# Optimization experiments

Measured on AMD Instinct MI355X. Metric: run time of the kernel, lower is better.

The kernel has to match this reference:

```python
import jax, jax.numpy as jnp
import numpy as np

N, C, H, W, Z = 2, 12, 128, 128, 128
SMOOTH = 1e-5  # MONAI DiceLoss smooth_nr / smooth_dr defaults
BETA = 3.0


def setup_inputs() -> dict:
    key = jax.random.key(0)
    k1, k2, k3 = jax.random.split(key, 3)
    inp = jax.random.normal(k1, (N, C, H, W, Z), dtype=jnp.float32)
    tgt = jax.random.randint(k2, (N, 1, H, W, Z), 0, C, dtype=jnp.int64)
    mat = jax.random.uniform(k3, (C, C), dtype=jnp.float32)
    return {"input": inp, "target": tgt, "matrix_penalty": mat}


def reference(input, target, matrix_penalty):
    c = input.shape[1]
    tgt = target[:, 0]  # (n,h,w,z) integer labels

    # ---- CE part of DiceCELoss (softmax cross-entropy, mean reduction) ----
    logp = jax.nn.log_softmax(input, axis=1)            # (n,c,h,w,z)
    ce = -jnp.mean(jnp.take_along_axis(logp, target, axis=1))

    # ---- Dice part (to_onehot_y=True, softmax=True, include_background) ----
    p = jnp.exp(logp)                                    # softmax probs
    t1h = jax.nn.one_hot(tgt, c, axis=1, dtype=p.dtype)  # (n,c,h,w,z)
    axes = (2, 3, 4)                                     # reduce spatial dims
    inter = jnp.sum(t1h * p, axis=axes)                  # (n,c)
    ground_o = jnp.sum(t1h, axis=axes)
    pred_o = jnp.sum(p, axis=axes)
    dice = jnp.mean(1.0 - (2.0 * inter + SMOOTH) / (ground_o + pred_o + SMOOTH))

    # ---- DOMINO penalty: mean over pixels of M[t,:] . softmax(logits) ----
    rows = matrix_penalty[tgt]                           # (n,h,w,z,c) gather
    p_last = jnp.moveaxis(p, 1, -1)                      # (n,h,w,z,c)
    penalty = BETA * jnp.mean(jnp.sum(rows * p_last, axis=-1))

    return ce + dice + penalty
```

## Files before the change

kernel.cpp:

```cpp
#include <hip/hip_runtime.h>

#define HWZ (128*128*128)
#define NN 2
#define CC 12
#define BLOCK 256
#define BLOCKS_PER_N 1024
#define GPT 4
#define NREP 8

static constexpr float SMOOTHF = 1e-5f;
static constexpr float BETAF   = 3.0f;


__global__ __launch_bounds__(BLOCK) void loss_main(
    const float* __restrict__ in, const int* __restrict__ tgt,
    const float* __restrict__ mat, float* __restrict__ ws)
{
    __shared__ float smat[CC * CC];
    __shared__ float red[4][38];
    const int tid = threadIdx.x;
    if (tid < CC * CC) smat[tid] = mat[tid];
    __syncthreads();

    const int n = blockIdx.y;
    const float* __restrict__ inb = in + (size_t)n * CC * HWZ;
    const int*   __restrict__ tb  = tgt + (size_t)n * HWZ;

    float ce = 0.f, pen = 0.f;
    float inter[CC], pred[CC];
    unsigned long long cnt_pack = 0ull;
    #pragma unroll
    for (int c = 0; c < CC; ++c) { inter[c] = 0.f; pred[c] = 0.f; }

    #pragma unroll 1
    for (int g = 0; g < GPT; ++g) {
        const int grp = g * (BLOCKS_PER_N * BLOCK) + blockIdx.x * BLOCK + tid;
        const size_t s = (size_t)grp * 2;

        float2 x[CC];
        #pragma unroll
        for (int c = 0; c < CC; ++c)
            x[c] = *reinterpret_cast<const float2*>(inb + (size_t)c * HWZ + s);
        const int2 t2 = *reinterpret_cast<const int2*>(tb + s);

        #pragma unroll
        for (int j = 0; j < 2; ++j) {
            float xv[CC];
            #pragma unroll
            for (int c = 0; c < CC; ++c) xv[c] = (j == 0) ? x[c].x : x[c].y;
            const int t = (j == 0) ? t2.x : t2.y;

            float e[CC], sum = 0.f;
            #pragma unroll
            for (int c = 0; c < CC; ++c) { e[c] = __expf(xv[c]); sum += e[c]; }
            const float inv = __builtin_amdgcn_rcpf(sum);
            const float lse = __logf(sum);

            float rw[CC];
            *reinterpret_cast<float4*>(&rw[0]) = *reinterpret_cast<const float4*>(&smat[t * CC + 0]);
            *reinterpret_cast<float4*>(&rw[4]) = *reinterpret_cast<const float4*>(&smat[t * CC + 4]);
            *reinterpret_cast<float4*>(&rw[8]) = *reinterpret_cast<const float4*>(&smat[t * CC + 8]);

            float xt = 0.f, pdot = 0.f;
            #pragma unroll
            for (int c = 0; c < CC; ++c) {
                const float p = e[c] * inv;
                pred[c] += p;
                const bool hit = (c == t);
                xt = hit ? xv[c] : xt;
                inter[c] += hit ? p : 0.f;
                pdot += rw[c] * p;
            }
            cnt_pack += 1ull << (t * 4);
            ce  += lse - xt;
            pen += pdot;
        }
    }

    float acc[38];
    acc[0] = ce; acc[1] = pen;
    #pragma unroll
    for (int c = 0; c < CC; ++c) {
        acc[2 + c]  = inter[c];
        acc[14 + c] = pred[c];
        acc[26 + c] = (float)((cnt_pack >> (c * 4)) & 15ull);
    }

    const int wave = tid >> 6;
    const int lane = tid & 63;
    #pragma unroll
    for (int k = 0; k < 38; ++k) {
        float v = acc[k];
        #pragma unroll
        for (int off = 32; off >= 1; off >>= 1)
            v += __shfl_xor(v, off, 64);
        if (lane == 0) red[wave][k] = v;
    }
    __syncthreads();

    if (tid < 38) {
        const float s4 = red[0][tid] + red[1][tid] + red[2][tid] + red[3][tid];
        int gidx;
        if (tid < 2)       gidx = tid;
        else if (tid < 14) gidx = 2  + n * CC + (tid - 2);
        else if (tid < 26) gidx = 26 + n * CC + (tid - 14);
        else               gidx = 50 + n * CC + (tid - 26);
        const int r = blockIdx.x & (NREP - 1);
        atomicAdd(&ws[r * 74 + gidx], s4);
    }
}

__global__ void loss_final(const float* __restrict__ ws, float* __restrict__ out)
{
    __shared__ float agg[74];
    const int tid = threadIdx.x;
    if (tid < 74) {
        float s = 0.f;
        #pragma unroll
        for (int r = 0; r < NREP; ++r) s += ws[r * 74 + tid];
        agg[tid] = s;
    }
    __syncthreads();
    if (tid == 0) {
        const float V = (float)((long)NN * HWZ);
        const float ce  = agg[0] / V;
        const float pen = BETAF * agg[1] / V;
        float dice = 0.f;
        for (int i = 0; i < NN * CC; ++i) {
            const float it = agg[2 + i], pr = agg[26 + i], ct = agg[50 + i];
            dice += 1.f - (2.f * it + SMOOTHF) / (ct + pr + SMOOTHF);
        }
        dice *= (1.0f / (NN * CC));
        out[0] = ce + dice + pen;
    }
}

extern "C" void kernel_launch(void* const* d_in, const int* in_sizes, int n_in,
                              void* d_out, int out_size, void* d_ws, size_t ws_size,
                              hipStream_t stream)
{
    const float* in  = (const float*)d_in[0];
    const int*   tgt = (const int*)d_in[1];
    const float* mat = (const float*)d_in[2];
    float* ws  = (float*)d_ws;
    float* out = (float*)d_out;

    hipMemsetAsync(ws, 0, NREP * 74 * sizeof(float), stream);
    dim3 grid(BLOCKS_PER_N, NN);
    loss_main<<<grid, BLOCK, 0, stream>>>(in, tgt, mat, ws);
    loss_final<<<1, 128, 0, stream>>>(ws, out);
}
```

Measured before the change: 62.41 us.

## Double-buffer input tiles into LDS via async global_load_lds prefetch

The main loop is restructured to stream 256-voxel tiles of all 12 channels into a double-buffered LDS area with global_load_lds. The next tile is prefetched while the current one is processed, using manual vmcnt waits and barriers. The grid becomes a persistent-style 768 blocks per batch striding over tiles, and each thread now handles one voxel per tile instead of float2 pairs. This is meant to hide global memory latency in a bandwidth-bound reduction. In exchange it adds two barriers per tile, LDS traffic, and hand-written waitcnt logic that relies on the compiler's load ordering.

Result: slower. 68.51 us (+9.8%).

```diff
diff --git a/kernel.cpp b/kernel.cpp
--- a/kernel.cpp
+++ b/kernel.cpp
@@ -4,23 +4,31 @@
 #define NN 2
 #define CC 12
 #define BLOCK 256
-#define BLOCKS_PER_N 1024
-#define GPT 4
+#define TV 256
+#define TILES (HWZ / TV)
+#define BX 768
 #define NREP 8
 
 static constexpr float SMOOTHF = 1e-5f;
 static constexpr float BETAF   = 3.0f;
+
+#define GLD16(gsrc, ldst) __builtin_amdgcn_global_load_lds( \
+  (const __attribute__((address_space(1))) void*)(gsrc),    \
+  (__attribute__((address_space(3))) void*)(ldst), 16, 0, 0)
 
 
 __global__ __launch_bounds__(BLOCK) void loss_main(
     const float* __restrict__ in, const int* __restrict__ tgt,
     const float* __restrict__ mat, float* __restrict__ ws)
 {
-    __shared__ float smat[CC * CC];
+    __shared__ __align__(16) float lds_in[2][CC][TV];
+    __shared__ __align__(16) float smat[CC * CC];
     __shared__ float red[4][38];
-    const int tid = threadIdx.x;
+
+    const int tid  = threadIdx.x;
+    const int wave = tid >> 6;
+    const int lane = tid & 63;
     if (tid < CC * CC) smat[tid] = mat[tid];
-    __syncthreads();
 
     const int n = blockIdx.y;
     const float* __restrict__ inb = in + (size_t)n * CC * HWZ;
@@ -32,49 +40,73 @@
     #pragma unroll
     for (int c = 0; c < CC; ++c) { inter[c] = 0.f; pred[c] = 0.f; }
 
+    __syncthreads();
+
+    int tile = blockIdx.x;
+    int p = 0;
+    int tcur = 0;
+    {
+        const int v0 = tile * TV;
+        #pragma unroll
+        for (int k = 0; k < 3; ++k) {
+            const int c = wave * 3 + k;
+            GLD16(inb + (size_t)c * HWZ + v0 + lane * 4, &lds_in[0][c][lane * 4]);
+        }
+        tcur = tb[v0 + tid];
+    }
+
     #pragma unroll 1
-    for (int g = 0; g < GPT; ++g) {
-        const int grp = g * (BLOCKS_PER_N * BLOCK) + blockIdx.x * BLOCK + tid;
-        const size_t s = (size_t)grp * 2;
+    for (; tile < TILES; tile += BX) {
+        const int nxt = tile + BX;
+        int tnext = 0;
+        if (nxt < TILES) {
+            const int v0n = nxt * TV;
+            #pragma unroll
+            for (int k = 0; k < 3; ++k) {
+                const int c = wave * 3 + k;
+                GLD16(inb + (size_t)c * HWZ + v0n + lane * 4, &lds_in[p ^ 1][c][lane * 4]);
+            }
+            tnext = tb[v0n + tid];
+            asm volatile("s_waitcnt vmcnt(4)" ::: "memory");
+        } else {
+            asm volatile("s_waitcnt vmcnt(0)" ::: "memory");
+        }
+        __builtin_amdgcn_s_barrier();
 
-        float2 x[CC];
+        const float* lbuf = &lds_in[p][0][0];
+        const int t = tcur;
+
+        float e[CC], xt = 0.f, sum = 0.f;
         #pragma unroll
-        for (int c = 0; c < CC; ++c)
-            x[c] = *reinterpret_cast<const float2*>(inb + (size_t)c * HWZ + s);
-        const int2 t2 = *reinterpret_cast<const int2*>(tb + s);
+        for (int c = 0; c < CC; ++c) {
+            const float x = lbuf[c * TV + tid];
+            xt = (c == t) ? x : xt;
+            e[c] = __expf(x);
+            sum += e[c];
+        }
+        const float inv = __builtin_amdgcn_rcpf(sum);
+        const float lse = __logf(sum);
 
+        float rw[CC];
+        *reinterpret_cast<float4*>(&rw[0]) = *reinterpret_cast<const float4*>(&smat[t * CC + 0]);
+        *reinterpret_cast<float4*>(&rw[4]) = *reinterpret_cast<const float4*>(&smat[t * CC + 4]);
+        *reinterpret_cast<float4*>(&rw[8]) = *reinterpret_cast<const float4*>(&smat[t * CC + 8]);
+
+        float pdot = 0.f;
         #pragma unroll
-        for (int j = 0; j < 2; ++j) {
-            float xv[CC];
-            #pragma unroll
-            for (int c = 0; c < CC; ++c) xv[c] = (j == 0) ? x[c].x : x[c].y;
-            const int t = (j == 0) ? t2.x : t2.y;
+        for (int c = 0; c < CC; ++c) {
+            const float pr = e[c] * inv;
+            pred[c]  += pr;
+            inter[c] += (c == t) ? pr : 0.f;
+            pdot += rw[c] * pr;
+        }
+        ce  += lse - xt;
+        pen += pdot;
+        cnt_pack += 1ull << (t * 4);
 
-            float e[CC], sum = 0.f;
-            #pragma unroll
-            for (int c = 0; c < CC; ++c) { e[c] = __expf(xv[c]); sum += e[c]; }
-            const float inv = __builtin_amdgcn_rcpf(sum);
-            const float lse = __logf(sum);
-
-            float rw[CC];
-            *reinterpret_cast<float4*>(&rw[0]) = *reinterpret_cast<const float4*>(&smat[t * CC + 0]);
-            *reinterpret_cast<float4*>(&rw[4]) = *reinterpret_cast<const float4*>(&smat[t * CC + 4]);
-            *reinterpret_cast<float4*>(&rw[8]) = *reinterpret_cast<const float4*>(&smat[t * CC + 8]);
-
-            float xt = 0.f, pdot = 0.f;
-            #pragma unroll
-            for (int c = 0; c < CC; ++c) {
-                const float p = e[c] * inv;
-                pred[c] += p;
-                const bool hit = (c == t);
-                xt = hit ? xv[c] : xt;
-                inter[c] += hit ? p : 0.f;
-                pdot += rw[c] * p;
-            }
-            cnt_pack += 1ull << (t * 4);
-            ce  += lse - xt;
-            pen += pdot;
-        }
+        __builtin_amdgcn_s_barrier();
+        p ^= 1;
+        tcur = tnext;
     }
 
     float acc[38];
@@ -86,8 +118,6 @@
         acc[26 + c] = (float)((cnt_pack >> (c * 4)) & 15ull);
     }
 
-    const int wave = tid >> 6;
-    const int lane = tid & 63;
     #pragma unroll
     for (int k = 0; k < 38; ++k) {
         float v = acc[k];
@@ -146,7 +176,7 @@
     float* out = (float*)d_out;
 
     hipMemsetAsync(ws, 0, NREP * 74 * sizeof(float), stream);
-    dim3 grid(BLOCKS_PER_N, NN);
+    dim3 grid(BX, NN);
     loss_main<<<grid, BLOCK, 0, stream>>>(in, tgt, mat, ws);
     loss_final<<<1, 128, 0, stream>>>(ws, out);
 }
```
